# Optimization experiments

Hardware: AMD Instinct MI355X
Metric: run time of the kernel (lower is better)

The kernel has to match this reference:

```python
import jax, jax.numpy as jnp
import numpy as np

N_NODES = 100_000
N_EDGES = 1_600_000
N_GRAPHS = 32
D_IN = 64
D_H1 = 64
D_H2 = 64
D_OUT = 10


def setup_inputs() -> dict:
    key = jax.random.key(0)
    ks = jax.random.split(key, 6)
    x = jax.random.normal(ks[0], (N_NODES, D_IN), dtype=jnp.float32)
    edge_index = jax.random.randint(ks[1], (2, N_EDGES), 0, N_NODES, dtype=jnp.int32)
    edge_weight = jax.random.uniform(ks[2], (N_EDGES,), dtype=jnp.float32)
    # deterministic sorted graph assignment: every one of the 32 graphs nonempty
    batch = ((jnp.arange(N_NODES) * N_GRAPHS) // N_NODES).astype(jnp.int32)
    W1 = jax.random.normal(ks[3], (D_IN, D_H1), dtype=jnp.float32) * 0.1
    b1 = jnp.zeros((D_H1,), dtype=jnp.float32)
    W2 = jax.random.normal(ks[4], (D_H1, D_H2), dtype=jnp.float32) * 0.1
    b2 = jnp.zeros((D_H2,), dtype=jnp.float32)
    Wlin = jax.random.normal(ks[5], (D_H2, D_OUT), dtype=jnp.float32) * 0.1
    blin = jnp.zeros((D_OUT,), dtype=jnp.float32)
    return {"x": x, "edge_index": edge_index, "edge_weight": edge_weight,
            "batch": batch, "W1": W1, "b1": b1, "W2": W2, "b2": b2,
            "Wlin": Wlin, "blin": blin}


def _gcn_norm(edge_index, edge_weight, n_nodes):
    """GCNConv(improved=True) normalization: add self-loops with weight 2.0,
    then norm_e = deg(dst)^-1/2 * w_e * deg(src)^-1/2."""
    loop = jnp.arange(n_nodes, dtype=edge_index.dtype)
    src = jnp.concatenate([edge_index[0], loop])
    dst = jnp.concatenate([edge_index[1], loop])
    w = jnp.concatenate([edge_weight, jnp.full((n_nodes,), 2.0, edge_weight.dtype)])
    deg = jax.ops.segment_sum(w, dst, num_segments=n_nodes)
    dinv = jnp.where(deg > 0, jax.lax.rsqrt(deg), 0.0)
    norm = dinv[src] * w * dinv[dst]
    return src, dst, norm


def _gcn_conv(h, W, b, src, dst, norm, n_nodes):
    hw = h @ W                                   # [N, d_out] transform first
    msg = hw[src] * norm[:, None]                # gather + scale  [E+N, d_out]
    return jax.ops.segment_sum(msg, dst, num_segments=n_nodes) + b


def reference(x, edge_index, edge_weight, batch, W1, b1, W2, b2, Wlin, blin):
    n = x.shape[0]
    src, dst, norm = _gcn_norm(edge_index, edge_weight, n)
    h = jax.nn.relu(_gcn_conv(x, W1, b1, src, dst, norm, n))
    h = jax.nn.relu(_gcn_conv(h, W2, b2, src, dst, norm, n))
    pooled = jax.ops.segment_max(h, batch, num_segments=N_GRAPHS)  # [G, d_h2]
    return pooled @ Wlin + blin
```

## Files before the change

kernel.cpp:

```cpp
#include <hip/hip_runtime.h>

#define N_NODES 100000
#define N_GRAPHS 32
#define N_EDGES 1600000
#define NODES_PER_GRAPH 3125
#define D 64
#define DOUT 10
#define CAP 64
#define PARTS 8
#define PART_NODES 12500
#define NCHUNK 782
#define CHUNK_EDGES 2048
#define EDGE_BLOCKS (PARTS * NCHUNK)
#define GEMM_BLOCKS 6250
#define WQ 32767.0f
#define POOL_SLICES 16

__device__ __forceinline__ unsigned short f2bf(float x) {
    unsigned u = __float_as_uint(x);
    u += 0x7FFFu + ((u >> 16) & 1u);
    return (unsigned short)(u >> 16);
}
__device__ __forceinline__ float bf2f(unsigned short h) {
    return __uint_as_float((unsigned)h << 16);
}
__device__ __forceinline__ float bflo(unsigned u) { return __uint_as_float(u << 16); }
__device__ __forceinline__ float bfhi(unsigned u) { return __uint_as_float(u & 0xFFFF0000u); }

__global__ void k_init(int* cnt, unsigned int* pooled) {
    int i = blockIdx.x * blockDim.x + threadIdx.x;
    if (i < N_NODES) cnt[i] = 0;
    if (i < N_GRAPHS * D) pooled[i] = 0u;
}

__global__ void k_fill_gemm(const int* __restrict__ src, const int* __restrict__ dst,
                            const float* __restrict__ w, int* cnt,
                            unsigned int* __restrict__ bucket,
                            const float* __restrict__ X, const float* __restrict__ W,
                            unsigned short* __restrict__ Y) {
    __shared__ float4 Ws[64 * 16];
    if (blockIdx.x < EDGE_BLOCKS) {
        int p = blockIdx.x & 7;
        int chunk = blockIdx.x >> 3;
        int base = chunk * CHUNK_EDGES;
        int lo = p * PART_NODES, hi = lo + PART_NODES;
#pragma unroll
        for (int j = 0; j < 8; ++j) {
            int e = base + j * 256 + threadIdx.x;
            if (e < N_EDGES) {
                int d = dst[e];
                if (d >= lo && d < hi) {
                    int pos = atomicAdd(&cnt[d], 1);
                    if (pos < CAP) {
                        unsigned int wq = (unsigned int)(w[e] * WQ + 0.5f);
                        bucket[d * CAP + pos] = ((unsigned int)src[e] << 15) | wq;
                    }
                }
            }
        }
    } else {
        int t = threadIdx.x;
        const float4* W4 = (const float4*)W;
        for (int i = t; i < 1024; i += 256) Ws[i] = W4[i];
        __syncthreads();
        int row = (blockIdx.x - EDGE_BLOCKS) * 16 + (t >> 4);
        int c4 = t & 15;
        const float4* xr4 = (const float4*)(X + (size_t)row * D);
        float4 acc = {0.f, 0.f, 0.f, 0.f};
#pragma unroll
        for (int k4 = 0; k4 < 16; ++k4) {
            float4 xv = xr4[k4];
            float4 w0 = Ws[(k4 * 4 + 0) * 16 + c4];
            float4 w1 = Ws[(k4 * 4 + 1) * 16 + c4];
            float4 w2 = Ws[(k4 * 4 + 2) * 16 + c4];
            float4 w3 = Ws[(k4 * 4 + 3) * 16 + c4];
            acc.x += xv.x * w0.x + xv.y * w1.x + xv.z * w2.x + xv.w * w3.x;
            acc.y += xv.x * w0.y + xv.y * w1.y + xv.z * w2.y + xv.w * w3.y;
            acc.z += xv.x * w0.z + xv.y * w1.z + xv.z * w2.z + xv.w * w3.z;
            acc.w += xv.x * w0.w + xv.y * w1.w + xv.z * w2.w + xv.w * w3.w;
        }
        ushort4 o;
        o.x = f2bf(acc.x); o.y = f2bf(acc.y); o.z = f2bf(acc.z); o.w = f2bf(acc.w);
        ((ushort4*)Y)[(size_t)row * 16 + c4] = o;
    }
}

__global__ void k_deg(const int* __restrict__ cnt, const unsigned int* __restrict__ bucket,
                      float* __restrict__ dinv) {
    int node = blockIdx.x * 4 + (threadIdx.x >> 6);
    int lane = threadIdx.x & 63;
    int c = cnt[node];
    if (c > CAP) c = CAP;
    float wv = 0.0f;
    if (lane < c) wv = (float)(bucket[node * CAP + lane] & 32767u);
#pragma unroll
    for (int off = 1; off < 64; off <<= 1) wv += __shfl_xor(wv, off);
    if (lane == 0) dinv[node] = rsqrtf(2.0f + wv * (1.0f / WQ));
}

__global__ void k_gemm64v(const float* __restrict__ X, const float* __restrict__ W,
                          unsigned short* __restrict__ Y) {
    __shared__ float4 Ws[64 * 16];
    int t = threadIdx.x;
    const float4* W4 = (const float4*)W;
    for (int i = t; i < 1024; i += 256) Ws[i] = W4[i];
    __syncthreads();
    int row = blockIdx.x * 16 + (t >> 4);
    int c4 = t & 15;
    const float4* xr4 = (const float4*)(X + (size_t)row * D);
    float4 acc = {0.f, 0.f, 0.f, 0.f};
#pragma unroll
    for (int k4 = 0; k4 < 16; ++k4) {
        float4 xv = xr4[k4];
        float4 w0 = Ws[(k4 * 4 + 0) * 16 + c4];
        float4 w1 = Ws[(k4 * 4 + 1) * 16 + c4];
        float4 w2 = Ws[(k4 * 4 + 2) * 16 + c4];
        float4 w3 = Ws[(k4 * 4 + 3) * 16 + c4];
        acc.x += xv.x * w0.x + xv.y * w1.x + xv.z * w2.x + xv.w * w3.x;
        acc.y += xv.x * w0.y + xv.y * w1.y + xv.z * w2.y + xv.w * w3.y;
        acc.z += xv.x * w0.z + xv.y * w1.z + xv.z * w2.z + xv.w * w3.z;
        acc.w += xv.x * w0.w + xv.y * w1.w + xv.z * w2.w + xv.w * w3.w;
    }
    ushort4 o;
    o.x = f2bf(acc.x); o.y = f2bf(acc.y); o.z = f2bf(acc.z); o.w = f2bf(acc.w);
    ((ushort4*)Y)[(size_t)row * 16 + c4] = o;
}

#define GATHER_BODY                                                              \
    int node = blockIdx.x * 4 + (threadIdx.x >> 6);                              \
    int lane = threadIdx.x & 63;                                                 \
    int g = lane >> 3, q = lane & 7;                                             \
    int end = cnt[node];                                                         \
    if (end > CAP) end = CAP;                                                    \
    float dvd = dinv[node];                                                      \
    float wsc = dvd * (1.0f / WQ);                                               \
    const unsigned int* bk = bucket + node * CAP;                                \
    float a0=0.f,a1=0.f,a2=0.f,a3=0.f,a4=0.f,a5=0.f,a6=0.f,a7=0.f;               \
    if (g == 0) {                                      \
        float s = 2.0f * dvd * dvd;                                              \
        uint4 u = hw8[(size_t)node * 8 + q];                                     \
        a0 = bflo(u.x)*s; a1 = bfhi(u.x)*s; a2 = bflo(u.y)*s; a3 = bfhi(u.y)*s;  \
        a4 = bflo(u.z)*s; a5 = bfhi(u.z)*s; a6 = bflo(u.w)*s; a7 = bfhi(u.w)*s;  \
    }                                                                            \
    int e = g;                                                                   \
    for (; e + 8 < end; e += 16) {                                               \
        unsigned int e0 = bk[e];                                                 \
        unsigned int e1 = bk[e + 8];                                             \
        int s0 = e0 >> 15, s1 = e1 >> 15;                                        \
        float d0 = dinv[s0], d1 = dinv[s1];                                      \
        uint4 u0 = hw8[(size_t)s0 * 8 + q];                                      \
        uint4 u1 = hw8[(size_t)s1 * 8 + q];                                      \
        float n0 = d0 * (float)(e0 & 32767u) * wsc;                              \
        float n1 = d1 * (float)(e1 & 32767u) * wsc;                              \
        a0 += bflo(u0.x)*n0 + bflo(u1.x)*n1; a1 += bfhi(u0.x)*n0 + bfhi(u1.x)*n1;\
        a2 += bflo(u0.y)*n0 + bflo(u1.y)*n1; a3 += bfhi(u0.y)*n0 + bfhi(u1.y)*n1;\
        a4 += bflo(u0.z)*n0 + bflo(u1.z)*n1; a5 += bfhi(u0.z)*n0 + bfhi(u1.z)*n1;\
        a6 += bflo(u0.w)*n0 + bflo(u1.w)*n1; a7 += bfhi(u0.w)*n0 + bfhi(u1.w)*n1;\
    }                                                                            \
    for (; e < end; e += 8) {                                                    \
        unsigned int ee = bk[e];                                                 \
        int s = ee >> 15;                                                        \
        float nrm = dinv[s] * (float)(ee & 32767u) * wsc;                        \
        uint4 u = hw8[(size_t)s * 8 + q];                                        \
        a0 += bflo(u.x)*nrm; a1 += bfhi(u.x)*nrm;                                \
        a2 += bflo(u.y)*nrm; a3 += bfhi(u.y)*nrm;                                \
        a4 += bflo(u.z)*nrm; a5 += bfhi(u.z)*nrm;                                \
        a6 += bflo(u.w)*nrm; a7 += bfhi(u.w)*nrm;                                \
    }                                                                            \
                            \
    a0 += __shfl_xor(a0, 8);  a1 += __shfl_xor(a1, 8);                           \
    a2 += __shfl_xor(a2, 8);  a3 += __shfl_xor(a3, 8);                           \
    a4 += __shfl_xor(a4, 8);  a5 += __shfl_xor(a5, 8);                           \
    a6 += __shfl_xor(a6, 8);  a7 += __shfl_xor(a7, 8);                           \
    a0 += __shfl_xor(a0, 16); a1 += __shfl_xor(a1, 16);                          \
    a2 += __shfl_xor(a2, 16); a3 += __shfl_xor(a3, 16);                          \
    a4 += __shfl_xor(a4, 16); a5 += __shfl_xor(a5, 16);                          \
    a6 += __shfl_xor(a6, 16); a7 += __shfl_xor(a7, 16);                          \
    a0 += __shfl_xor(a0, 32); a1 += __shfl_xor(a1, 32);                          \
    a2 += __shfl_xor(a2, 32); a3 += __shfl_xor(a3, 32);                          \
    a4 += __shfl_xor(a4, 32); a5 += __shfl_xor(a5, 32);                          \
    a6 += __shfl_xor(a6, 32); a7 += __shfl_xor(a7, 32);

__global__ void k_gather8_f32(const int* __restrict__ cnt, const unsigned int* __restrict__ bucket,
                              const uint4* __restrict__ hw8, const float* __restrict__ dinv,
                              const float* __restrict__ b, float4* __restrict__ out4) {
    GATHER_BODY
    if (g == 0) {
        float4 b0 = ((const float4*)b)[2 * q];
        float4 b1 = ((const float4*)b)[2 * q + 1];
        float4 r0, r1;
        r0.x = fmaxf(a0 + b0.x, 0.f); r0.y = fmaxf(a1 + b0.y, 0.f);
        r0.z = fmaxf(a2 + b0.z, 0.f); r0.w = fmaxf(a3 + b0.w, 0.f);
        r1.x = fmaxf(a4 + b1.x, 0.f); r1.y = fmaxf(a5 + b1.y, 0.f);
        r1.z = fmaxf(a6 + b1.z, 0.f); r1.w = fmaxf(a7 + b1.w, 0.f);
        out4[(size_t)node * 16 + 2 * q] = r0;
        out4[(size_t)node * 16 + 2 * q + 1] = r1;
    }
}

__global__ void k_gather8_bf16(const int* __restrict__ cnt, const unsigned int* __restrict__ bucket,
                               const uint4* __restrict__ hw8, const float* __restrict__ dinv,
                               const float* __restrict__ b, uint4* __restrict__ outb) {
    GATHER_BODY
    if (g == 0) {
        float4 b0 = ((const float4*)b)[2 * q];
        float4 b1 = ((const float4*)b)[2 * q + 1];
        uint4 r;
        r.x = (unsigned)f2bf(fmaxf(a0 + b0.x, 0.f)) | ((unsigned)f2bf(fmaxf(a1 + b0.y, 0.f)) << 16);
        r.y = (unsigned)f2bf(fmaxf(a2 + b0.z, 0.f)) | ((unsigned)f2bf(fmaxf(a3 + b0.w, 0.f)) << 16);
        r.z = (unsigned)f2bf(fmaxf(a4 + b1.x, 0.f)) | ((unsigned)f2bf(fmaxf(a5 + b1.y, 0.f)) << 16);
        r.w = (unsigned)f2bf(fmaxf(a6 + b1.z, 0.f)) | ((unsigned)f2bf(fmaxf(a7 + b1.w, 0.f)) << 16);
        outb[(size_t)node * 8 + q] = r;
    }
}

__global__ void k_pool(const unsigned short* __restrict__ h, unsigned int* pooled) {
    __shared__ float s[256];
    int g = blockIdx.x / POOL_SLICES;
    int slice = blockIdx.x % POOL_SLICES;
    int t = threadIdx.x;
    int f = t & 63, r = t >> 6;
    float m = 0.0f;
    size_t base = (size_t)g * NODES_PER_GRAPH;
    for (int i = slice * 4 + r; i < NODES_PER_GRAPH; i += 4 * POOL_SLICES)
        m = fmaxf(m, bf2f(h[(base + i) * D + f]));
    s[t] = m;
    __syncthreads();
    if (t < 128) s[t] = fmaxf(s[t], s[t + 128]);
    __syncthreads();
    if (t < 64) atomicMax(&pooled[g * D + t], __float_as_uint(fmaxf(s[t], s[t + 64])));
}

__global__ void k_final(const float* __restrict__ pooled, const float* __restrict__ Wlin,
                        const float* __restrict__ blin, float* __restrict__ out) {
    int t = threadIdx.x;
    if (t < N_GRAPHS * DOUT) {
        int g = t / DOUT, o = t % DOUT;
        float acc = blin[o];
#pragma unroll
        for (int f = 0; f < D; ++f) acc += pooled[g * D + f] * Wlin[f * DOUT + o];
        out[t] = acc;
    }
}

extern "C" void kernel_launch(void* const* d_in, const int* in_sizes, int n_in,
                              void* d_out, int out_size, void* d_ws, size_t ws_size,
                              hipStream_t stream) {
    const float* x     = (const float*)d_in[0];
    const int*   ei    = (const int*)d_in[1];
    const int*   src   = ei;
    const int*   dst   = ei + N_EDGES;
    const float* ew    = (const float*)d_in[2];
    const float* W1    = (const float*)d_in[4];
    const float* b1    = (const float*)d_in[5];
    const float* W2    = (const float*)d_in[6];
    const float* b2    = (const float*)d_in[7];
    const float* Wlin  = (const float*)d_in[8];
    const float* blin  = (const float*)d_in[9];
    float* out = (float*)d_out;

    unsigned int* bucket = (unsigned int*)d_ws;
    float* h1     = (float*)(bucket + (size_t)N_NODES * CAP);
    unsigned short* hwA = (unsigned short*)(h1 + (size_t)N_NODES * D);
    unsigned short* hwB = hwA + (size_t)N_NODES * D;
    unsigned short* h2  = hwB + (size_t)N_NODES * D;
    float* dinv   = (float*)(h2 + (size_t)N_NODES * D);
    float* pooled = dinv + N_NODES;
    int*   cnt    = (int*)(pooled + N_GRAPHS * D);

    const int B = 256;
    int gN = (N_NODES + B - 1) / B;

    k_init<<<gN, B, 0, stream>>>(cnt, (unsigned int*)pooled);
    k_fill_gemm<<<EDGE_BLOCKS + GEMM_BLOCKS, B, 0, stream>>>(src, dst, ew, cnt, bucket, x, W1, hwA);
    k_deg<<<N_NODES / 4, B, 0, stream>>>(cnt, bucket, dinv);

    k_gather8_f32<<<N_NODES / 4, B, 0, stream>>>(cnt, bucket, (const uint4*)hwA, dinv, b1, (float4*)h1);
    k_gemm64v<<<GEMM_BLOCKS, B, 0, stream>>>(h1, W2, hwB);
    k_gather8_bf16<<<N_NODES / 4, B, 0, stream>>>(cnt, bucket, (const uint4*)hwB, dinv, b2, (uint4*)h2);

    k_pool<<<N_GRAPHS * POOL_SLICES, B, 0, stream>>>(h2, (unsigned int*)pooled);
    k_final<<<1, 320, 0, stream>>>(pooled, Wlin, blin, out);
}
```

Before: 324.2 us.

## Fuse layer-1 gather with layer-2 GEMM and fold final linear into pooling

The first aggregation kernel now applies bias and ReLU, then multiplies by W2 from shared memory using wave shuffles and writes bf16 directly. This removes the fp32 h1 round trip and the separate GEMM launch. Pooling and the final linear layer are merged into one kernel, where the last-finishing block, detected with an atomic counter, computes the output. This saves a launch but adds per-wave shuffle and FMA work and a serialized tail in a single block.

```diff
diff --git a/kernel.cpp b/kernel.cpp
--- a/kernel.cpp
+++ b/kernel.cpp
@@ -15,6 +15,7 @@
 #define GEMM_BLOCKS 6250
 #define WQ 32767.0f
 #define POOL_SLICES 16
+#define POOL_BLOCKS (N_GRAPHS * POOL_SLICES)
 
 __device__ __forceinline__ unsigned short f2bf(float x) {
     unsigned u = __float_as_uint(x);
@@ -30,7 +31,7 @@
 __global__ void k_init(int* cnt, unsigned int* pooled) {
     int i = blockIdx.x * blockDim.x + threadIdx.x;
     if (i < N_NODES) cnt[i] = 0;
-    if (i < N_GRAPHS * D) pooled[i] = 0u;
+    if (i < N_GRAPHS * D + 1) pooled[i] = 0u;
 }
 
 __global__ void k_fill_gemm(const int* __restrict__ src, const int* __restrict__ dst,
@@ -98,36 +99,8 @@
     if (lane == 0) dinv[node] = rsqrtf(2.0f + wv * (1.0f / WQ));
 }
 
-__global__ void k_gemm64v(const float* __restrict__ X, const float* __restrict__ W,
-                          unsigned short* __restrict__ Y) {
-    __shared__ float4 Ws[64 * 16];
-    int t = threadIdx.x;
-    const float4* W4 = (const float4*)W;
-    for (int i = t; i < 1024; i += 256) Ws[i] = W4[i];
-    __syncthreads();
-    int row = blockIdx.x * 16 + (t >> 4);
-    int c4 = t & 15;
-    const float4* xr4 = (const float4*)(X + (size_t)row * D);
-    float4 acc = {0.f, 0.f, 0.f, 0.f};
-#pragma unroll
-    for (int k4 = 0; k4 < 16; ++k4) {
-        float4 xv = xr4[k4];
-        float4 w0 = Ws[(k4 * 4 + 0) * 16 + c4];
-        float4 w1 = Ws[(k4 * 4 + 1) * 16 + c4];
-        float4 w2 = Ws[(k4 * 4 + 2) * 16 + c4];
-        float4 w3 = Ws[(k4 * 4 + 3) * 16 + c4];
-        acc.x += xv.x * w0.x + xv.y * w1.x + xv.z * w2.x + xv.w * w3.x;
-        acc.y += xv.x * w0.y + xv.y * w1.y + xv.z * w2.y + xv.w * w3.y;
-        acc.z += xv.x * w0.z + xv.y * w1.z + xv.z * w2.z + xv.w * w3.z;
-        acc.w += xv.x * w0.w + xv.y * w1.w + xv.z * w2.w + xv.w * w3.w;
-    }
-    ushort4 o;
-    o.x = f2bf(acc.x); o.y = f2bf(acc.y); o.z = f2bf(acc.z); o.w = f2bf(acc.w);
-    ((ushort4*)Y)[(size_t)row * 16 + c4] = o;
-}
-
-#define GATHER_BODY                                                              \
-    int node = blockIdx.x * 4 + (threadIdx.x >> 6);                              \
+#define GATHER_BODY(NPB)                                                         \
+    int node = blockIdx.x * NPB + (threadIdx.x >> 6);                            \
     int lane = threadIdx.x & 63;                                                 \
     int g = lane >> 3, q = lane & 7;                                             \
     int end = cnt[node];                                                         \
@@ -167,7 +140,7 @@
         a4 += bflo(u.z)*nrm; a5 += bfhi(u.z)*nrm;                                \
         a6 += bflo(u.w)*nrm; a7 += bfhi(u.w)*nrm;                                \
     }                                                                            \
-                            \
+            \
     a0 += __shfl_xor(a0, 8);  a1 += __shfl_xor(a1, 8);                           \
     a2 += __shfl_xor(a2, 8);  a3 += __shfl_xor(a3, 8);                           \
     a4 += __shfl_xor(a4, 8);  a5 += __shfl_xor(a5, 8);                           \
@@ -181,27 +154,43 @@
     a4 += __shfl_xor(a4, 32); a5 += __shfl_xor(a5, 32);                          \
     a6 += __shfl_xor(a6, 32); a7 += __shfl_xor(a7, 32);
 
-__global__ void k_gather8_f32(const int* __restrict__ cnt, const unsigned int* __restrict__ bucket,
+__global__ void k_gather_gemm(const int* __restrict__ cnt, const unsigned int* __restrict__ bucket,
                               const uint4* __restrict__ hw8, const float* __restrict__ dinv,
-                              const float* __restrict__ b, float4* __restrict__ out4) {
-    GATHER_BODY
-    if (g == 0) {
-        float4 b0 = ((const float4*)b)[2 * q];
-        float4 b1 = ((const float4*)b)[2 * q + 1];
-        float4 r0, r1;
-        r0.x = fmaxf(a0 + b0.x, 0.f); r0.y = fmaxf(a1 + b0.y, 0.f);
-        r0.z = fmaxf(a2 + b0.z, 0.f); r0.w = fmaxf(a3 + b0.w, 0.f);
-        r1.x = fmaxf(a4 + b1.x, 0.f); r1.y = fmaxf(a5 + b1.y, 0.f);
-        r1.z = fmaxf(a6 + b1.z, 0.f); r1.w = fmaxf(a7 + b1.w, 0.f);
-        out4[(size_t)node * 16 + 2 * q] = r0;
-        out4[(size_t)node * 16 + 2 * q + 1] = r1;
-    }
+                              const float* __restrict__ b1, const float* __restrict__ W2,
+                              unsigned short* __restrict__ outB) {
+    __shared__ float W2s[64 * 64];
+    {
+        int t = threadIdx.x;
+        float4* d4 = (float4*)W2s;
+        const float4* s4 = (const float4*)W2;
+        for (int i = t; i < 1024; i += 512) d4[i] = s4[i];
+    }
+    __syncthreads();
+    GATHER_BODY(8)
+    float4 bb0 = ((const float4*)b1)[2 * q];
+    float4 bb1 = ((const float4*)b1)[2 * q + 1];
+    float u0 = fmaxf(a0 + bb0.x, 0.f), u1 = fmaxf(a1 + bb0.y, 0.f);
+    float u2 = fmaxf(a2 + bb0.z, 0.f), u3 = fmaxf(a3 + bb0.w, 0.f);
+    float u4 = fmaxf(a4 + bb1.x, 0.f), u5 = fmaxf(a5 + bb1.y, 0.f);
+    float u6 = fmaxf(a6 + bb1.z, 0.f), u7 = fmaxf(a7 + bb1.w, 0.f);
+    float y = 0.f;
+#pragma unroll
+    for (int qq = 0; qq < 8; ++qq) {
+        float t0 = __shfl(u0, qq), t1 = __shfl(u1, qq);
+        float t2 = __shfl(u2, qq), t3 = __shfl(u3, qq);
+        float t4 = __shfl(u4, qq), t5 = __shfl(u5, qq);
+        float t6 = __shfl(u6, qq), t7 = __shfl(u7, qq);
+        const float* wr = &W2s[(qq * 8) * 64 + lane];
+        y += t0 * wr[0]   + t1 * wr[64]  + t2 * wr[128] + t3 * wr[192]
+           + t4 * wr[256] + t5 * wr[320] + t6 * wr[384] + t7 * wr[448];
+    }
+    outB[(size_t)node * D + lane] = f2bf(y);
 }
 
 __global__ void k_gather8_bf16(const int* __restrict__ cnt, const unsigned int* __restrict__ bucket,
                                const uint4* __restrict__ hw8, const float* __restrict__ dinv,
                                const float* __restrict__ b, uint4* __restrict__ outb) {
-    GATHER_BODY
+    GATHER_BODY(4)
     if (g == 0) {
         float4 b0 = ((const float4*)b)[2 * q];
         float4 b1 = ((const float4*)b)[2 * q + 1];
@@ -214,32 +203,53 @@
     }
 }
 
-__global__ void k_pool(const unsigned short* __restrict__ h, unsigned int* pooled) {
-    __shared__ float s[256];
+__global__ void k_pool_final(const unsigned short* __restrict__ h,
+                             unsigned int* __restrict__ pooled,
+                             const float* __restrict__ Wlin,
+                             const float* __restrict__ blin,
+                             float* __restrict__ out) {
+    __shared__ float2 s[256];
+    __shared__ float sp[N_GRAPHS * D];
+    __shared__ int isLast;
     int g = blockIdx.x / POOL_SLICES;
     int slice = blockIdx.x % POOL_SLICES;
     int t = threadIdx.x;
-    int f = t & 63, r = t >> 6;
-    float m = 0.0f;
-    size_t base = (size_t)g * NODES_PER_GRAPH;
-    for (int i = slice * 4 + r; i < NODES_PER_GRAPH; i += 4 * POOL_SLICES)
-        m = fmaxf(m, bf2f(h[(base + i) * D + f]));
-    s[t] = m;
-    __syncthreads();
-    if (t < 128) s[t] = fmaxf(s[t], s[t + 128]);
-    __syncthreads();
-    if (t < 64) atomicMax(&pooled[g * D + t], __float_as_uint(fmaxf(s[t], s[t + 64])));
-}
-
-__global__ void k_final(const float* __restrict__ pooled, const float* __restrict__ Wlin,
-                        const float* __restrict__ blin, float* __restrict__ out) {
-    int t = threadIdx.x;
-    if (t < N_GRAPHS * DOUT) {
-        int g = t / DOUT, o = t % DOUT;
-        float acc = blin[o];
-#pragma unroll
-        for (int f = 0; f < D; ++f) acc += pooled[g * D + f] * Wlin[f * DOUT + o];
-        out[t] = acc;
+    int f2 = t & 31;
+    int r = t >> 5;
+    float m0 = 0.0f, m1 = 0.0f;
+    const unsigned int* hu = (const unsigned int*)(h + (size_t)g * NODES_PER_GRAPH * D);
+    for (int i = slice * 8 + r; i < NODES_PER_GRAPH; i += 8 * POOL_SLICES) {
+        unsigned int u = hu[(size_t)i * 32 + f2];
+        m0 = fmaxf(m0, bflo(u));
+        m1 = fmaxf(m1, bfhi(u));
+    }
+    s[t].x = m0; s[t].y = m1;
+    __syncthreads();
+    if (t < 128) { s[t].x = fmaxf(s[t].x, s[t + 128].x); s[t].y = fmaxf(s[t].y, s[t + 128].y); }
+    __syncthreads();
+    if (t < 64)  { s[t].x = fmaxf(s[t].x, s[t + 64].x);  s[t].y = fmaxf(s[t].y, s[t + 64].y); }
+    __syncthreads();
+    if (t < 32) {
+        atomicMax(&pooled[g * D + 2 * t],     __float_as_uint(fmaxf(s[t].x, s[t + 32].x)));
+        atomicMax(&pooled[g * D + 2 * t + 1], __float_as_uint(fmaxf(s[t].y, s[t + 32].y)));
+    }
+    __threadfence();
+    __syncthreads();
+    if (t == 0) {
+        unsigned int* done = pooled + N_GRAPHS * D;
+        isLast = (atomicAdd(done, 1u) == POOL_BLOCKS - 1);
+    }
+    __syncthreads();
+    if (!isLast) return;
+    for (int i = t; i < N_GRAPHS * D; i += 256)
+        sp[i] = __uint_as_float(atomicMax(&pooled[i], 0u));
+    __syncthreads();
+    for (int o = t; o < N_GRAPHS * DOUT; o += 256) {
+        int gg = o / DOUT, oo = o % DOUT;
+        float acc = blin[oo];
+#pragma unroll
+        for (int f = 0; f < D; ++f) acc += sp[gg * D + f] * Wlin[f * DOUT + oo];
+        out[o] = acc;
     }
 }
 
@@ -260,25 +270,22 @@
     float* out = (float*)d_out;
 
     unsigned int* bucket = (unsigned int*)d_ws;
-    float* h1     = (float*)(bucket + (size_t)N_NODES * CAP);
-    unsigned short* hwA = (unsigned short*)(h1 + (size_t)N_NODES * D);
+    unsigned short* hwA = (unsigned short*)(bucket + (size_t)N_NODES * CAP);
     unsigned short* hwB = hwA + (size_t)N_NODES * D;
     unsigned short* h2  = hwB + (size_t)N_NODES * D;
     float* dinv   = (float*)(h2 + (size_t)N_NODES * D);
-    float* pooled = dinv + N_NODES;
-    int*   cnt    = (int*)(pooled + N_GRAPHS * D);
+    unsigned int* pooled = (unsigned int*)(dinv + N_NODES);
+    int*   cnt    = (int*)(pooled + N_GRAPHS * D + 1);
 
     const int B = 256;
     int gN = (N_NODES + B - 1) / B;
 
-    k_init<<<gN, B, 0, stream>>>(cnt, (unsigned int*)pooled);
+    k_init<<<gN, B, 0, stream>>>(cnt, pooled);
     k_fill_gemm<<<EDGE_BLOCKS + GEMM_BLOCKS, B, 0, stream>>>(src, dst, ew, cnt, bucket, x, W1, hwA);
     k_deg<<<N_NODES / 4, B, 0, stream>>>(cnt, bucket, dinv);
 
-    k_gather8_f32<<<N_NODES / 4, B, 0, stream>>>(cnt, bucket, (const uint4*)hwA, dinv, b1, (float4*)h1);
-    k_gemm64v<<<GEMM_BLOCKS, B, 0, stream>>>(h1, W2, hwB);
+    k_gather_gemm<<<N_NODES / 8, 512, 0, stream>>>(cnt, bucket, (const uint4*)hwA, dinv, b1, W2, hwB);
     k_gather8_bf16<<<N_NODES / 4, B, 0, stream>>>(cnt, bucket, (const uint4*)hwB, dinv, b2, (uint4*)h2);
 
-    k_pool<<<N_GRAPHS * POOL_SLICES, B, 0, stream>>>(h2, (unsigned int*)pooled);
-    k_final<<<1, 320, 0, stream>>>(pooled, Wlin, blin, out);
-}
+    k_pool_final<<<POOL_BLOCKS, B, 0, stream>>>(h2, pooled, Wlin, blin, out);
+}
```

After: 409.6 us. +26.3%, slower.

## Preload bucket edges per lane with shuffles and fuse pool with final linear

Applied to the files above, without the earlier changes.

In the gather kernels each lane now loads one bucket entry and computes its normalization once, and the feature-gathering lanes read source index and weight through wavefront shuffles instead of repeating the bucket and dinv loads. Pooling is vectorized to read bf16 pairs, and the final linear layer is folded into the pool kernel using a last-block-done atomic counter, which removes one launch. The change adds shuffle traffic and threadfence/atomic synchronization, and relies on the done counter being zeroed by the init kernel on every call.

```diff
diff --git a/kernel.cpp b/kernel.cpp
--- a/kernel.cpp
+++ b/kernel.cpp
@@ -15,6 +15,7 @@
 #define GEMM_BLOCKS 6250
 #define WQ 32767.0f
 #define POOL_SLICES 16
+#define POOL_BLOCKS (N_GRAPHS * POOL_SLICES)
 
 __device__ __forceinline__ unsigned short f2bf(float x) {
     unsigned u = __float_as_uint(x);
@@ -30,7 +31,7 @@
 __global__ void k_init(int* cnt, unsigned int* pooled) {
     int i = blockIdx.x * blockDim.x + threadIdx.x;
     if (i < N_NODES) cnt[i] = 0;
-    if (i < N_GRAPHS * D) pooled[i] = 0u;
+    if (i < N_GRAPHS * D + 1) pooled[i] = 0u;
 }
 
 __global__ void k_fill_gemm(const int* __restrict__ src, const int* __restrict__ dst,
@@ -98,76 +99,52 @@
     if (lane == 0) dinv[node] = rsqrtf(2.0f + wv * (1.0f / WQ));
 }
 
-__global__ void k_gemm64v(const float* __restrict__ X, const float* __restrict__ W,
-                          unsigned short* __restrict__ Y) {
-    __shared__ float4 Ws[64 * 16];
-    int t = threadIdx.x;
-    const float4* W4 = (const float4*)W;
-    for (int i = t; i < 1024; i += 256) Ws[i] = W4[i];
-    __syncthreads();
-    int row = blockIdx.x * 16 + (t >> 4);
-    int c4 = t & 15;
-    const float4* xr4 = (const float4*)(X + (size_t)row * D);
-    float4 acc = {0.f, 0.f, 0.f, 0.f};
-#pragma unroll
-    for (int k4 = 0; k4 < 16; ++k4) {
-        float4 xv = xr4[k4];
-        float4 w0 = Ws[(k4 * 4 + 0) * 16 + c4];
-        float4 w1 = Ws[(k4 * 4 + 1) * 16 + c4];
-        float4 w2 = Ws[(k4 * 4 + 2) * 16 + c4];
-        float4 w3 = Ws[(k4 * 4 + 3) * 16 + c4];
-        acc.x += xv.x * w0.x + xv.y * w1.x + xv.z * w2.x + xv.w * w3.x;
-        acc.y += xv.x * w0.y + xv.y * w1.y + xv.z * w2.y + xv.w * w3.y;
-        acc.z += xv.x * w0.z + xv.y * w1.z + xv.z * w2.z + xv.w * w3.z;
-        acc.w += xv.x * w0.w + xv.y * w1.w + xv.z * w2.w + xv.w * w3.w;
-    }
-    ushort4 o;
-    o.x = f2bf(acc.x); o.y = f2bf(acc.y); o.z = f2bf(acc.z); o.w = f2bf(acc.w);
-    ((ushort4*)Y)[(size_t)row * 16 + c4] = o;
-}
-
 #define GATHER_BODY                                                              \
     int node = blockIdx.x * 4 + (threadIdx.x >> 6);                              \
     int lane = threadIdx.x & 63;                                                 \
     int g = lane >> 3, q = lane & 7;                                             \
-    int end = cnt[node];                                                         \
-    if (end > CAP) end = CAP;                                                    \
+    int c = cnt[node];                                                           \
+    if (c > CAP) c = CAP;                                                        \
     float dvd = dinv[node];                                                      \
     float wsc = dvd * (1.0f / WQ);                                               \
     const unsigned int* bk = bucket + node * CAP;                                \
+    unsigned int ee = (lane < c) ? bk[lane] : 0u;                                \
+    int s_l = (lane < c) ? (int)(ee >> 15) : 0;                                  \
+    float nrm_l = (lane < c) ? dinv[s_l] * (float)(ee & 32767u) * wsc : 0.0f;    \
     float a0=0.f,a1=0.f,a2=0.f,a3=0.f,a4=0.f,a5=0.f,a6=0.f,a7=0.f;               \
-    if (g == 0) {                                      \
+    if (g == 0) {        \
         float s = 2.0f * dvd * dvd;                                              \
         uint4 u = hw8[(size_t)node * 8 + q];                                     \
         a0 = bflo(u.x)*s; a1 = bfhi(u.x)*s; a2 = bflo(u.y)*s; a3 = bfhi(u.y)*s;  \
         a4 = bflo(u.z)*s; a5 = bfhi(u.z)*s; a6 = bflo(u.w)*s; a7 = bfhi(u.w)*s;  \
     }                                                                            \
-    int e = g;                                                                   \
-    for (; e + 8 < end; e += 16) {                                               \
-        unsigned int e0 = bk[e];                                                 \
-        unsigned int e1 = bk[e + 8];                                             \
-        int s0 = e0 >> 15, s1 = e1 >> 15;                                        \
-        float d0 = dinv[s0], d1 = dinv[s1];                                      \
+    int nt = (c + 7) >> 3;                          \
+    int t = 0;                                                                   \
+    for (; t + 1 < nt; t += 2) {     \
+        int e0 = g + 8 * t;                       \
+        int e1 = e0 + 8;                  \
+        int s0 = __shfl(s_l, e0);                                                \
+        int s1 = __shfl(s_l, e1);                                                \
+        float n0 = __shfl(nrm_l, e0);                                            \
+        float n1 = __shfl(nrm_l, e1);                                            \
         uint4 u0 = hw8[(size_t)s0 * 8 + q];                                      \
         uint4 u1 = hw8[(size_t)s1 * 8 + q];                                      \
-        float n0 = d0 * (float)(e0 & 32767u) * wsc;                              \
-        float n1 = d1 * (float)(e1 & 32767u) * wsc;                              \
         a0 += bflo(u0.x)*n0 + bflo(u1.x)*n1; a1 += bfhi(u0.x)*n0 + bfhi(u1.x)*n1;\
         a2 += bflo(u0.y)*n0 + bflo(u1.y)*n1; a3 += bfhi(u0.y)*n0 + bfhi(u1.y)*n1;\
         a4 += bflo(u0.z)*n0 + bflo(u1.z)*n1; a5 += bfhi(u0.z)*n0 + bfhi(u1.z)*n1;\
         a6 += bflo(u0.w)*n0 + bflo(u1.w)*n1; a7 += bfhi(u0.w)*n0 + bfhi(u1.w)*n1;\
     }                                                                            \
-    for (; e < end; e += 8) {                                                    \
-        unsigned int ee = bk[e];                                                 \
-        int s = ee >> 15;                                                        \
-        float nrm = dinv[s] * (float)(ee & 32767u) * wsc;                        \
+    if (t < nt) {                                         \
+        int e = g + 8 * t;                                                       \
+        int s = __shfl(s_l, e);                                                  \
+        float nrm = __shfl(nrm_l, e);                         \
         uint4 u = hw8[(size_t)s * 8 + q];                                        \
         a0 += bflo(u.x)*nrm; a1 += bfhi(u.x)*nrm;                                \
         a2 += bflo(u.y)*nrm; a3 += bfhi(u.y)*nrm;                                \
         a4 += bflo(u.z)*nrm; a5 += bfhi(u.z)*nrm;                                \
         a6 += bflo(u.w)*nrm; a7 += bfhi(u.w)*nrm;                                \
     }                                                                            \
-                            \
+                              \
     a0 += __shfl_xor(a0, 8);  a1 += __shfl_xor(a1, 8);                           \
     a2 += __shfl_xor(a2, 8);  a3 += __shfl_xor(a3, 8);                           \
     a4 += __shfl_xor(a4, 8);  a5 += __shfl_xor(a5, 8);                           \
@@ -214,32 +191,81 @@
     }
 }
 
-__global__ void k_pool(const unsigned short* __restrict__ h, unsigned int* pooled) {
-    __shared__ float s[256];
+__global__ void k_gemm64v(const float* __restrict__ X, const float* __restrict__ W,
+                          unsigned short* __restrict__ Y) {
+    __shared__ float4 Ws[64 * 16];
+    int t = threadIdx.x;
+    const float4* W4 = (const float4*)W;
+    for (int i = t; i < 1024; i += 256) Ws[i] = W4[i];
+    __syncthreads();
+    int row = blockIdx.x * 16 + (t >> 4);
+    int c4 = t & 15;
+    const float4* xr4 = (const float4*)(X + (size_t)row * D);
+    float4 acc = {0.f, 0.f, 0.f, 0.f};
+#pragma unroll
+    for (int k4 = 0; k4 < 16; ++k4) {
+        float4 xv = xr4[k4];
+        float4 w0 = Ws[(k4 * 4 + 0) * 16 + c4];
+        float4 w1 = Ws[(k4 * 4 + 1) * 16 + c4];
+        float4 w2 = Ws[(k4 * 4 + 2) * 16 + c4];
+        float4 w3 = Ws[(k4 * 4 + 3) * 16 + c4];
+        acc.x += xv.x * w0.x + xv.y * w1.x + xv.z * w2.x + xv.w * w3.x;
+        acc.y += xv.x * w0.y + xv.y * w1.y + xv.z * w2.y + xv.w * w3.y;
+        acc.z += xv.x * w0.z + xv.y * w1.z + xv.z * w2.z + xv.w * w3.z;
+        acc.w += xv.x * w0.w + xv.y * w1.w + xv.z * w2.w + xv.w * w3.w;
+    }
+    ushort4 o;
+    o.x = f2bf(acc.x); o.y = f2bf(acc.y); o.z = f2bf(acc.z); o.w = f2bf(acc.w);
+    ((ushort4*)Y)[(size_t)row * 16 + c4] = o;
+}
+
+__global__ void k_pool_final(const unsigned short* __restrict__ h,
+                             unsigned int* __restrict__ pooled,
+                             const float* __restrict__ Wlin,
+                             const float* __restrict__ blin,
+                             float* __restrict__ out) {
+    __shared__ float2 s[256];
+    __shared__ float sp[N_GRAPHS * D];
+    __shared__ int isLast;
     int g = blockIdx.x / POOL_SLICES;
     int slice = blockIdx.x % POOL_SLICES;
     int t = threadIdx.x;
-    int f = t & 63, r = t >> 6;
-    float m = 0.0f;
-    size_t base = (size_t)g * NODES_PER_GRAPH;
-    for (int i = slice * 4 + r; i < NODES_PER_GRAPH; i += 4 * POOL_SLICES)
-        m = fmaxf(m, bf2f(h[(base + i) * D + f]));
-    s[t] = m;
-    __syncthreads();
-    if (t < 128) s[t] = fmaxf(s[t], s[t + 128]);
-    __syncthreads();
-    if (t < 64) atomicMax(&pooled[g * D + t], __float_as_uint(fmaxf(s[t], s[t + 64])));
-}
-
-__global__ void k_final(const float* __restrict__ pooled, const float* __restrict__ Wlin,
-                        const float* __restrict__ blin, float* __restrict__ out) {
-    int t = threadIdx.x;
-    if (t < N_GRAPHS * DOUT) {
-        int g = t / DOUT, o = t % DOUT;
-        float acc = blin[o];
-#pragma unroll
-        for (int f = 0; f < D; ++f) acc += pooled[g * D + f] * Wlin[f * DOUT + o];
-        out[t] = acc;
+    int f2 = t & 31;
+    int r = t >> 5;
+    float m0 = 0.0f, m1 = 0.0f;
+    const unsigned int* hu = (const unsigned int*)(h + (size_t)g * NODES_PER_GRAPH * D);
+    for (int i = slice * 8 + r; i < NODES_PER_GRAPH; i += 8 * POOL_SLICES) {
+        unsigned int u = hu[(size_t)i * 32 + f2];
+        m0 = fmaxf(m0, bflo(u));
+        m1 = fmaxf(m1, bfhi(u));
+    }
+    s[t].x = m0; s[t].y = m1;
+    __syncthreads();
+    if (t < 128) { s[t].x = fmaxf(s[t].x, s[t + 128].x); s[t].y = fmaxf(s[t].y, s[t + 128].y); }
+    __syncthreads();
+    if (t < 64)  { s[t].x = fmaxf(s[t].x, s[t + 64].x);  s[t].y = fmaxf(s[t].y, s[t + 64].y); }
+    __syncthreads();
+    if (t < 32) {
+        atomicMax(&pooled[g * D + 2 * t],     __float_as_uint(fmaxf(s[t].x, s[t + 32].x)));
+        atomicMax(&pooled[g * D + 2 * t + 1], __float_as_uint(fmaxf(s[t].y, s[t + 32].y)));
+    }
+    __threadfence();
+    __syncthreads();
+    if (t == 0) {
+        unsigned int* done = pooled + N_GRAPHS * D;
+        isLast = (atomicAdd(done, 1u) == POOL_BLOCKS - 1);
+    }
+    __syncthreads();
+    if (!isLast) return;
+    for (int i = t; i < N_GRAPHS * D; i += 256)
+        sp[i] = __uint_as_float(atomicMax(&pooled[i], 0u));
+    __syncthreads();
+    for (int o = t; o < N_GRAPHS * DOUT; o += 256) {
+        int gg = o / DOUT, oo = o % DOUT;
+        float acc = blin[oo];
+#pragma unroll
+        for (int f = 0; f < D; ++f) acc += sp[gg * D + f] * Wlin[f * DOUT + oo];
+        out[o] = acc;
     }
 }
 
@@ -265,13 +291,13 @@
     unsigned short* hwB = hwA + (size_t)N_NODES * D;
     unsigned short* h2  = hwB + (size_t)N_NODES * D;
     float* dinv   = (float*)(h2 + (size_t)N_NODES * D);
-    float* pooled = dinv + N_NODES;
-    int*   cnt    = (int*)(pooled + N_GRAPHS * D);
+    unsigned int* pooled = (unsigned int*)(dinv + N_NODES);
+    int*   cnt    = (int*)(pooled + N_GRAPHS * D + 1);
 
     const int B = 256;
     int gN = (N_NODES + B - 1) / B;
 
-    k_init<<<gN, B, 0, stream>>>(cnt, (unsigned int*)pooled);
+    k_init<<<gN, B, 0, stream>>>(cnt, pooled);
     k_fill_gemm<<<EDGE_BLOCKS + GEMM_BLOCKS, B, 0, stream>>>(src, dst, ew, cnt, bucket, x, W1, hwA);
     k_deg<<<N_NODES / 4, B, 0, stream>>>(cnt, bucket, dinv);
 
@@ -279,6 +305,5 @@
     k_gemm64v<<<GEMM_BLOCKS, B, 0, stream>>>(h1, W2, hwB);
     k_gather8_bf16<<<N_NODES / 4, B, 0, stream>>>(cnt, bucket, (const uint4*)hwB, dinv, b2, (uint4*)h2);
 
-    k_pool<<<N_GRAPHS * POOL_SLICES, B, 0, stream>>>(h2, (unsigned int*)pooled);
-    k_final<<<1, 320, 0, stream>>>(pooled, Wlin, blin, out);
-}
+    k_pool_final<<<POOL_BLOCKS, B, 0, stream>>>(h2, pooled, Wlin, blin, out);
+}
```

New measurement: 365.1 us. 12.6% more time.
